# Performance work log

Measured on AMD Instinct MI355X. Metric: run time of the kernel, lower is better.

The kernel has to match this reference:

```python
import jax, jax.numpy as jnp
import numpy as np
import math

WINDOW = 512
N_HEAD = 16

def setup_inputs() -> dict:
    key = jax.random.key(0)
    ks = jax.random.split(key, 5)
    B, L, D = 2, 4096, 1024
    s = 0.02
    return {
        "x": jax.random.normal(ks[0], (B, L, D), dtype=jnp.float32),
        "Wq": jax.random.normal(ks[1], (D, D), dtype=jnp.float32) * s,
        "bq": jnp.zeros((D,), jnp.float32),
        "Wk": jax.random.normal(ks[2], (D, D), dtype=jnp.float32) * s,
        "bk": jnp.zeros((D,), jnp.float32),
        "Wv": jax.random.normal(ks[3], (D, D), dtype=jnp.float32) * s,
        "bv": jnp.zeros((D,), jnp.float32),
        "Wo": jax.random.normal(ks[4], (D, D), dtype=jnp.float32) * s,
        "bo": jnp.zeros((D,), jnp.float32),
    }

def reference(x, Wq, bq, Wk, bk, Wv, bv, Wo, bo):
    # Chunked sliding-window MHA (eval mode, dropout inactive).
    B, L, D = x.shape
    W, H = WINDOW, N_HEAD
    dh = D // H
    C = L // W  # number of query chunks
    scale = 1.0 / math.sqrt(dh)

    # Project full sequence once (linear, per-token -> identical math).
    q = x @ Wq.T + bq
    k = x @ Wk.T + bk
    v = x @ Wv.T + bv

    # Pad K/V by one window at the front so every chunk sees 2W keys.
    kp = jnp.pad(k, ((0, 0), (W, 0), (0, 0)))
    vp = jnp.pad(v, ((0, 0), (W, 0), (0, 0)))
    idx = jnp.arange(C)[:, None] * W + jnp.arange(2 * W)[None, :]  # [C, 2W] into padded seq
    kc = kp[:, idx].reshape(B, C, 2 * W, H, dh)
    vc = vp[:, idx].reshape(B, C, 2 * W, H, dh)
    qc = q.reshape(B, C, W, H, dh)

    scores = jnp.einsum('bcqhd,bckhd->bchqk', qc, kc) * scale  # [B,C,H,W,2W]
    valid = (idx >= W)  # padded positions (chunk 0's lookback) are invalid
    scores = jnp.where(valid[None, :, None, None, :], scores, jnp.float32(-1e9))
    attn = jax.nn.softmax(scores, axis=-1)
    out = jnp.einsum('bchqk,bckhd->bcqhd', attn, vc).reshape(B, L, D)
    return out @ Wo.T + bo
```

## Files before the change

kernel.cpp:

```cpp
#include <hip/hip_runtime.h>
#include <hip/hip_bf16.h>

typedef __hip_bfloat16 bf16;
typedef __attribute__((ext_vector_type(8))) short bf16x8;
typedef __attribute__((ext_vector_type(4))) float f32x4;
typedef unsigned int u32;
typedef unsigned short u16;

#define MFMA(a,b,c) __builtin_amdgcn_mfma_f32_16x16x32_bf16((a),(b),(c),0,0,0)

__device__ __forceinline__ u16 f32_to_bf16_rtne(float f) {
  u32 b = __builtin_bit_cast(u32, f);
  b += 0x7FFFu + ((b >> 16) & 1u);
  return (u16)(b >> 16);
}
__device__ __forceinline__ u32 pk2bf(float a, float b) {
  u32 ua = __builtin_bit_cast(u32, a); ua += 0x7FFFu + ((ua >> 16) & 1u);
  u32 ub = __builtin_bit_cast(u32, b); ub += 0x7FFFu + ((ub >> 16) & 1u);
  return __builtin_amdgcn_perm(ub, ua, 0x07060302u);
}
__device__ __forceinline__ u32 pk2bf_rtz(float a, float b) {
  return __builtin_amdgcn_perm(__builtin_bit_cast(u32, b),
                               __builtin_bit_cast(u32, a), 0x07060302u);
}
__device__ __forceinline__ uint4 cvt8(uint4 lo, uint4 hi) {
  const float4 fl = __builtin_bit_cast(float4, lo);
  const float4 fh = __builtin_bit_cast(float4, hi);
  uint4 r;
  r.x = pk2bf(fl.x, fl.y); r.y = pk2bf(fl.z, fl.w);
  r.z = pk2bf(fh.x, fh.y); r.w = pk2bf(fh.z, fh.w);
  return r;
}

__device__ __forceinline__ void barrier_lgkm() {
  asm volatile("s_waitcnt lgkmcnt(0)\n\ts_barrier" ::: "memory");
}

typedef const __attribute__((address_space(1))) void* gas_ptr;
typedef __attribute__((address_space(3))) void* las_ptr;
__device__ __forceinline__ void gload_lds16(const void* g, void* l) {
  __builtin_amdgcn_global_load_lds((gas_ptr)g, (las_ptr)l, 16, 0, 0);
}

static constexpr float SL2E = 0.125f * 1.44269504f;

__global__ __launch_bounds__(256)
void cast_all(const float* __restrict__ wq, const float* __restrict__ wk,
              const float* __restrict__ wv, const float* __restrict__ wo,
              const float* __restrict__ x,
              u16* __restrict__ wqkv, u16* __restrict__ wob,
              u16* __restrict__ xb) {
  const size_t DD8 = (size_t)1024 * 1024 / 8;
  if (blockIdx.x < 2048) {
    const int m = blockIdx.x >> 9;
    const size_t i = ((size_t)(blockIdx.x & 511)) * 256 + threadIdx.x;
    const float* src = (m == 0) ? wq : (m == 1) ? wk : (m == 2) ? wv : wo;
    u16* dst = (m < 3) ? (wqkv + (size_t)m * DD8 * 8) : wob;
    const float4* s = (const float4*)src + i * 2;
    ((uint4*)dst)[i] = cvt8(__builtin_bit_cast(uint4, s[0]),
                            __builtin_bit_cast(uint4, s[1]));
  } else {
    const size_t i = ((size_t)(blockIdx.x - 2048)) * 256 + threadIdx.x;
    const float4* s = (const float4*)x + i * 2;
    ((uint4*)xb)[i] = cvt8(__builtin_bit_cast(uint4, s[0]),
                           __builtin_bit_cast(uint4, s[1]));
  }
}

template <int MODE>
__global__ __launch_bounds__(256)
void gemm_bt(const bf16* __restrict__ A, const bf16* __restrict__ W,
             const float* __restrict__ b0, const float* __restrict__ b1,
             const float* __restrict__ b2, void* __restrict__ o0,
             void* __restrict__ o1, void* __restrict__ o2,
             int M, int N, int K)
{
  __shared__ bf16 As[128 * 64];
  __shared__ bf16 Bs[128 * 64];

  const int tid  = threadIdx.x;
  const int wave = tid >> 6, lane = tid & 63;
  const int quad = lane >> 4, l16 = lane & 15;
  const int wm   = wave >> 1, wn  = wave & 1;
  const int m0   = blockIdx.x * 128, n0 = blockIdx.y * 128;

  const int band = n0 >> 10;
  const float* bias = (band == 0) ? b0 : (band == 1) ? b1 : b2;

  const int srow = lane >> 3;
  const int sg   = lane & 7;
  const size_t rgs = (size_t)8 * K;
  const bf16* aSrc = A + (size_t)(m0 + wave * 32 + srow) * K + ((sg ^ srow) * 8);
  const bf16* wSrc = W + (size_t)(n0 + wave * 32 + srow) * K + ((sg ^ srow) * 8);
  bf16* aB = As + wave * 32 * 64;
  bf16* wB = Bs + wave * 32 * 64;

  const int niter = K >> 6;

  f32x4 acc[4][4] = {};

  const int arow[4] = { (wm * 64 + 0 * 16 + l16) * 64, (wm * 64 + 1 * 16 + l16) * 64,
                        (wm * 64 + 2 * 16 + l16) * 64, (wm * 64 + 3 * 16 + l16) * 64 };
  const int brow[4] = { (wn * 64 + 0 * 16 + l16) * 64, (wn * 64 + 1 * 16 + l16) * 64,
                        (wn * 64 + 2 * 16 + l16) * 64, (wn * 64 + 3 * 16 + l16) * 64 };
  const int r7 = l16 & 7;

  for (int t = 0; t < niter; ++t) {
    gload_lds16(aSrc,            aB);
    gload_lds16(aSrc + rgs,      aB + 512);
    gload_lds16(aSrc + 2 * rgs,  aB + 1024);
    gload_lds16(aSrc + 3 * rgs,  aB + 1536);
    gload_lds16(wSrc,            wB);
    gload_lds16(wSrc + rgs,      wB + 512);
    gload_lds16(wSrc + 2 * rgs,  wB + 1024);
    gload_lds16(wSrc + 3 * rgs,  wB + 1536);
    aSrc += 64; wSrc += 64;
    __syncthreads();

#pragma unroll
    for (int kk = 0; kk < 2; ++kk) {
      bf16x8 af[4], bw[4];
#pragma unroll
      for (int mt = 0; mt < 4; ++mt)
        af[mt] = *(const bf16x8*)(As + arow[mt] + (((kk * 4 + quad) ^ r7) * 8));
#pragma unroll
      for (int nt = 0; nt < 4; ++nt)
        bw[nt] = *(const bf16x8*)(Bs + brow[nt] + (((kk * 4 + quad) ^ r7) * 8));
#pragma unroll
      for (int mt = 0; mt < 4; ++mt)
#pragma unroll
        for (int nt = 0; nt < 4; ++nt)
          acc[mt][nt] = MFMA(af[mt], bw[nt], acc[mt][nt]);
    }
    if (t + 1 < niter) __syncthreads();
  }

#pragma unroll
  for (int nt = 0; nt < 4; ++nt) {
    const int col = n0 + wn * 64 + nt * 16 + l16;
    const int cl  = col & 1023;
    const float bv = bias[cl];
#pragma unroll
    for (int mt = 0; mt < 4; ++mt) {
      const int rbase = m0 + wm * 64 + mt * 16 + quad * 4;
      if (MODE == 1) {
#pragma unroll
        for (int r = 0; r < 4; ++r)
          ((float*)o0)[(size_t)(rbase + r) * N + col] = acc[mt][nt][r] + bv;
      } else if (band == 2) {
        const int hh = cl >> 6, dd = cl & 63;
        const int bb = rbase >> 12, tl = rbase & 4095;
        u16* dst = (u16*)o2 + ((size_t)((bb * 16 + hh) * 64 + dd)) * 4096 + tl;
        uint2 pk;
        pk.x = pk2bf(acc[mt][nt][0] + bv, acc[mt][nt][1] + bv);
        pk.y = pk2bf(acc[mt][nt][2] + bv, acc[mt][nt][3] + bv);
        *(uint2*)dst = pk;
      } else {
        u16* dst = (u16*)((band == 0) ? o0 : o1);
        const float sc = (band == 0) ? SL2E : 1.0f;
#pragma unroll
        for (int r = 0; r < 4; ++r)
          dst[(size_t)(rbase + r) * 1024 + cl] =
              f32_to_bf16_rtne((acc[mt][nt][r] + bv) * sc);
      }
    }
  }
}

__global__ __launch_bounds__(256)
void attn_swin(const bf16* __restrict__ qb, const bf16* __restrict__ kb,
               const bf16* __restrict__ vtb, u16* __restrict__ ctx)
{
  __shared__ __align__(16) bf16 Ks[2][64 * 72];
  __shared__ __align__(16) bf16 Vts[2][64 * 72];

  int bid = blockIdx.x;
  const int g  = bid & 255, qt = bid >> 8;
  const int h  = g & 15, c = (g >> 4) & 7, b = g >> 7;

  const int tid  = threadIdx.x;
  const int w    = tid >> 6, lane = tid & 63;
  const int quad = lane >> 4, l16 = lane & 15;

  const int tq0  = c * 512 + qt * 128;
  const int hoff = h * 64;
  const int kstart = (c == 0) ? 0 : (c - 1) * 512;
  const int nkt    = (c == 0) ? 8 : 16;

  bf16x8 qf[2][2];
#pragma unroll
  for (int u = 0; u < 2; ++u) {
    const bf16* qr = qb + ((size_t)(b * 4096 + tq0 + w * 32 + u * 16 + l16)) * 1024 + hoff;
    qf[u][0] = *(const bf16x8*)(qr + quad * 8);
    qf[u][1] = *(const bf16x8*)(qr + 32 + quad * 8);
  }

  const int m    = tid >> 2;
  const int cseg = (tid & 3) * 16;
  const int sig  = (((m >> 4) & 1) << 5) | (((m >> 2) & 3) << 3)
                 | (((m >> 5) & 1) << 2) | (m & 3);
  const bf16* kgp = kb + ((size_t)(b * 4096 + kstart + sig)) * 1024 + hoff + cseg;
  const bf16* vgp = vtb + ((size_t)((b * 16 + h) * 64 + m)) * 4096 + kstart + cseg;
  const int soff = m * 72 + cseg;

  float l_i[2] = {0.f, 0.f};
  f32x4 o[2][4] = {};

  uint4 ka0 = *(const uint4*)(kgp), ka1 = *(const uint4*)(kgp + 8);
  uint4 va0 = *(const uint4*)(vgp), va1 = *(const uint4*)(vgp + 8);
  kgp += (size_t)64 * 1024; vgp += 64;
  *(uint4*)(Ks[0] + soff) = ka0; *(uint4*)(Ks[0] + soff + 8) = ka1;
  *(uint4*)(Vts[0] + soff) = va0; *(uint4*)(Vts[0] + soff + 8) = va1;
  ka0 = *(const uint4*)(kgp); ka1 = *(const uint4*)(kgp + 8);
  va0 = *(const uint4*)(vgp); va1 = *(const uint4*)(vgp + 8);
  kgp += (size_t)64 * 1024; vgp += 64;
  barrier_lgkm();

  typedef union { u32 d[4]; bf16x8 v; } fragu;

  auto compute = [&](const bf16* ksb, const bf16* vtsb) {
    f32x4 s[2][4] = {};
#pragma unroll
    for (int kt = 0; kt < 4; ++kt) {
      const bf16* kr = ksb + (kt * 16 + l16) * 72;
      bf16x8 kf0 = *(const bf16x8*)(kr + quad * 8);
      bf16x8 kf1 = *(const bf16x8*)(kr + 32 + quad * 8);
      s[0][kt] = MFMA(kf0, qf[0][0], s[0][kt]);
      s[0][kt] = MFMA(kf1, qf[0][1], s[0][kt]);
      s[1][kt] = MFMA(kf0, qf[1][0], s[1][kt]);
      s[1][kt] = MFMA(kf1, qf[1][1], s[1][kt]);
    }
    fragu pf[2][2];
#pragma unroll
    for (int u = 0; u < 2; ++u) {
      float rs = 0.f;
#pragma unroll
      for (int kt = 0; kt < 4; ++kt)
#pragma unroll
        for (int r = 0; r < 4; ++r) {
          const float p = __builtin_amdgcn_exp2f(s[u][kt][r]);
          s[u][kt][r] = p;
          rs += p;
        }
      rs += __shfl_xor(rs, 16);
      rs += __shfl_xor(rs, 32);
      l_i[u] += rs;
#pragma unroll
      for (int hh = 0; hh < 2; ++hh)
#pragma unroll
        for (int dw = 0; dw < 4; ++dw) {
          const int kt = 2 * (dw >> 1) + hh, r0 = 2 * (dw & 1);
          pf[u][hh].d[dw] = pk2bf_rtz(s[u][kt][r0], s[u][kt][r0 + 1]);
        }
    }
#pragma unroll
    for (int dt = 0; dt < 4; ++dt) {
      const bf16* vr = vtsb + (dt * 16 + l16) * 72;
      bf16x8 vf0 = *(const bf16x8*)(vr + quad * 8);
      bf16x8 vf1 = *(const bf16x8*)(vr + 32 + quad * 8);
      o[0][dt] = MFMA(vf0, pf[0][0].v, o[0][dt]);
      o[0][dt] = MFMA(vf1, pf[0][1].v, o[0][dt]);
      o[1][dt] = MFMA(vf0, pf[1][0].v, o[1][dt]);
      o[1][dt] = MFMA(vf1, pf[1][1].v, o[1][dt]);
    }
  };

  for (int t = 0; t < nkt; t += 2) {
    *(uint4*)(Ks[1] + soff) = ka0; *(uint4*)(Ks[1] + soff + 8) = ka1;
    *(uint4*)(Vts[1] + soff) = va0; *(uint4*)(Vts[1] + soff + 8) = va1;
    if (t + 2 < nkt) {
      ka0 = *(const uint4*)(kgp); ka1 = *(const uint4*)(kgp + 8);
      va0 = *(const uint4*)(vgp); va1 = *(const uint4*)(vgp + 8);
      kgp += (size_t)64 * 1024; vgp += 64;
    }
    compute(Ks[0], Vts[0]);
    barrier_lgkm();

    if (t + 2 < nkt) {
      *(uint4*)(Ks[0] + soff) = ka0; *(uint4*)(Ks[0] + soff + 8) = ka1;
      *(uint4*)(Vts[0] + soff) = va0; *(uint4*)(Vts[0] + soff + 8) = va1;
      if (t + 3 < nkt) {
        ka0 = *(const uint4*)(kgp); ka1 = *(const uint4*)(kgp + 8);
        va0 = *(const uint4*)(vgp); va1 = *(const uint4*)(vgp + 8);
        kgp += (size_t)64 * 1024; vgp += 64;
      }
    }
    compute(Ks[1], Vts[1]);
    barrier_lgkm();
  }

#pragma unroll
  for (int u = 0; u < 2; ++u) {
    const float inv = 1.0f / l_i[u];
    const int qrow = tq0 + w * 32 + u * 16 + l16;
    u16* crow = ctx + ((size_t)(b * 4096 + qrow)) * 1024 + hoff;
#pragma unroll
    for (int dt = 0; dt < 4; ++dt) {
      uint2 pk;
      pk.x = pk2bf(o[u][dt][0] * inv, o[u][dt][1] * inv);
      pk.y = pk2bf(o[u][dt][2] * inv, o[u][dt][3] * inv);
      *(uint2*)(crow + dt * 16 + quad * 4) = pk;
    }
  }
}

extern "C" void kernel_launch(void* const* d_in, const int* in_sizes, int n_in,
                              void* d_out, int out_size, void* d_ws, size_t ws_size,
                              hipStream_t stream) {
  const float* x  = (const float*)d_in[0];
  const float* Wq = (const float*)d_in[1];
  const float* bq = (const float*)d_in[2];
  const float* Wk = (const float*)d_in[3];
  const float* bk = (const float*)d_in[4];
  const float* Wv = (const float*)d_in[5];
  const float* bv = (const float*)d_in[6];
  const float* Wo = (const float*)d_in[7];
  const float* bo = (const float*)d_in[8];

  const size_t MD = (size_t)8192 * 1024;
  const size_t DD = (size_t)1024 * 1024;

  char* ws = (char*)d_ws;
  u16*  Wqkvb = (u16*)ws;                     ws += 3 * DD * 2;
  u16*  Wob   = (u16*)ws;                     ws += DD * 2;
  u16*  qbuf  = (u16*)ws;                     ws += MD * 2;
  u16*  kbuf  = (u16*)ws;                     ws += MD * 2;
  u16*  vtb   = (u16*)ws;                     ws += MD * 2;
  u16*  ctx   = (u16*)ws;

  u16* xb = ctx;

  cast_all<<<dim3(6144), dim3(256), 0, stream>>>(Wq, Wk, Wv, Wo, x,
                                                 Wqkvb, Wob, xb);

  gemm_bt<0><<<dim3(64, 24), dim3(256), 0, stream>>>(
      (const bf16*)xb, (const bf16*)Wqkvb, bq, bk, bv,
      qbuf, kbuf, vtb, 8192, 3072, 1024);

  attn_swin<<<dim3(1024), dim3(256), 0, stream>>>(
      (const bf16*)qbuf, (const bf16*)kbuf, (const bf16*)vtb, ctx);

  gemm_bt<1><<<dim3(64, 8), dim3(256), 0, stream>>>(
      (const bf16*)ctx, (const bf16*)Wob, bo, bo, bo,
      d_out, nullptr, nullptr, 8192, 1024, 1024);
}
```

Measured before the change: 240.0 us.

## Replace QKV projection GEMM with 256x256-tile double-buffered pipelined kernel

Adds a new QKV projection kernel that uses 256x256 output tiles with 512 threads and double-buffered LDS filled by direct global-to-LDS loads two k-steps ahead. Each k-step is split into four phases with staggered prefetch issues, s_setprio around the MFMA bursts, and an XCD-aware workgroup remap. The aim is to raise arithmetic intensity and overlap memory with MFMA work in the largest GEMM. The cost is much higher LDS use (128KB per block) and register pressure, and only 384 workgroups, which risks lower occupancy. The output GEMM is split into its own specialised kernel.

Result: slower. 257.1 us (+7.1%).

```diff
diff --git a/kernel.cpp b/kernel.cpp
--- a/kernel.cpp
+++ b/kernel.cpp
@@ -34,6 +34,15 @@
 
 __device__ __forceinline__ void barrier_lgkm() {
   asm volatile("s_waitcnt lgkmcnt(0)\n\ts_barrier" ::: "memory");
+}
+__device__ __forceinline__ void barrier_plain() {
+  asm volatile("s_barrier" ::: "memory");
+}
+__device__ __forceinline__ void barrier_vm8() {
+  asm volatile("s_waitcnt vmcnt(8)\n\ts_barrier" ::: "memory");
+}
+__device__ __forceinline__ void barrier_vm0() {
+  asm volatile("s_waitcnt vmcnt(0)\n\ts_barrier" ::: "memory");
 }
 
 typedef const __attribute__((address_space(1))) void* gas_ptr;
@@ -67,13 +76,176 @@
   }
 }
 
-template <int MODE>
+__global__ __launch_bounds__(512, 2)
+void gemm256_qkv(const bf16* __restrict__ A, const bf16* __restrict__ W,
+                 const float* __restrict__ b0, const float* __restrict__ b1,
+                 const float* __restrict__ b2,
+                 u16* __restrict__ o0, u16* __restrict__ o1, u16* __restrict__ o2,
+                 int M, int N, int K)
+{
+  __shared__ bf16 AsB[2][256 * 64];
+  __shared__ bf16 BsB[2][256 * 64];
+
+  int wg = blockIdx.y * gridDim.x + blockIdx.x;
+  const int q8 = (gridDim.x * gridDim.y) >> 3;
+  wg = (wg & 7) * q8 + (wg >> 3);
+  const int bx = wg & 31;
+  const int by = wg >> 5;
+  const int m0 = bx * 256, n0 = by * 256;
+
+  const int tid  = threadIdx.x;
+  const int wv   = tid >> 6, lane = tid & 63;
+  const int quad = lane >> 4, l16 = lane & 15;
+  const int wm   = wv >> 2, wn = wv & 3;
+  const int r7   = l16 & 7;
+
+  const int rr = tid >> 3, g = tid & 7;
+  const int sg8 = (g ^ (rr & 7)) * 8;
+  const bf16* aS = A + (size_t)(m0 + rr) * K + sg8;
+  const bf16* wS = W + (size_t)(n0 + rr) * K + sg8;
+  const int ldstW = wv * 8 * 64;
+
+#define STA(c, qk, kt) gload_lds16(aS + ((size_t)(qk) * 64) * K + (kt) * 64, \
+                                   &AsB[c][(qk) * 64 * 64 + ldstW])
+#define STB(c, qk, kt) gload_lds16(wS + ((size_t)(qk) * 64) * K + (kt) * 64, \
+                                   &BsB[c][(qk) * 64 * 64 + ldstW])
+
+  int aoff[8], boff[4];
+#pragma unroll
+  for (int mt = 0; mt < 8; ++mt) aoff[mt] = (wm * 128 + mt * 16 + l16) * 64;
+#pragma unroll
+  for (int nt = 0; nt < 4; ++nt) boff[nt] = (wn * 64 + nt * 16 + l16) * 64;
+  const int k0 = (quad ^ r7) * 8;
+  const int k1 = ((4 + quad) ^ r7) * 8;
+
+  f32x4 acc[8][4] = {};
+  bf16x8 af[4][2], bl[2][2], bh[2][2];
+
+  const int nk = K >> 6;
+
+#pragma unroll
+  for (int qk = 0; qk < 4; ++qk) { STA(0, qk, 0); STB(0, qk, 0); }
+#pragma unroll
+  for (int qk = 0; qk < 4; ++qk) { STA(1, qk, 1); STB(1, qk, 1); }
+  barrier_vm8();
+
+  for (int t = 0; t < nk; ++t) {
+    const int c = t & 1;
+    const bf16* Ac = AsB[c];
+    const bf16* Bc = BsB[c];
+    const int t2 = t + 2;
+    const bool pf = (t2 < nk);
+
+#pragma unroll
+    for (int mt = 0; mt < 4; ++mt) {
+      af[mt][0] = *(const bf16x8*)(Ac + aoff[mt] + k0);
+      af[mt][1] = *(const bf16x8*)(Ac + aoff[mt] + k1);
+    }
+#pragma unroll
+    for (int nt = 0; nt < 2; ++nt) {
+      bl[nt][0] = *(const bf16x8*)(Bc + boff[nt] + k0);
+      bl[nt][1] = *(const bf16x8*)(Bc + boff[nt] + k1);
+    }
+    barrier_plain();
+    __builtin_amdgcn_s_setprio(1);
+#pragma unroll
+    for (int mt = 0; mt < 4; ++mt)
+#pragma unroll
+      for (int nt = 0; nt < 2; ++nt) {
+        acc[mt][nt] = MFMA(af[mt][0], bl[nt][0], acc[mt][nt]);
+        acc[mt][nt] = MFMA(af[mt][1], bl[nt][1], acc[mt][nt]);
+      }
+    __builtin_amdgcn_s_setprio(0);
+    barrier_lgkm();
+
+#pragma unroll
+    for (int nt = 0; nt < 2; ++nt) {
+      bh[nt][0] = *(const bf16x8*)(Bc + boff[nt + 2] + k0);
+      bh[nt][1] = *(const bf16x8*)(Bc + boff[nt + 2] + k1);
+    }
+    if (pf) { STA(c, 0, t2); STA(c, 2, t2); }
+    barrier_plain();
+    __builtin_amdgcn_s_setprio(1);
+#pragma unroll
+    for (int mt = 0; mt < 4; ++mt)
+#pragma unroll
+      for (int nt = 0; nt < 2; ++nt) {
+        acc[mt][nt + 2] = MFMA(af[mt][0], bh[nt][0], acc[mt][nt + 2]);
+        acc[mt][nt + 2] = MFMA(af[mt][1], bh[nt][1], acc[mt][nt + 2]);
+      }
+    __builtin_amdgcn_s_setprio(0);
+    barrier_lgkm();
+
+#pragma unroll
+    for (int mt = 0; mt < 4; ++mt) {
+      af[mt][0] = *(const bf16x8*)(Ac + aoff[mt + 4] + k0);
+      af[mt][1] = *(const bf16x8*)(Ac + aoff[mt + 4] + k1);
+    }
+    if (pf) { STB(c, 0, t2); STB(c, 1, t2); }
+    barrier_plain();
+    __builtin_amdgcn_s_setprio(1);
+#pragma unroll
+    for (int mt = 0; mt < 4; ++mt)
+#pragma unroll
+      for (int nt = 0; nt < 2; ++nt) {
+        acc[mt + 4][nt + 2] = MFMA(af[mt][0], bh[nt][0], acc[mt + 4][nt + 2]);
+        acc[mt + 4][nt + 2] = MFMA(af[mt][1], bh[nt][1], acc[mt + 4][nt + 2]);
+      }
+    __builtin_amdgcn_s_setprio(0);
+    barrier_lgkm();
+
+    if (pf) { STA(c, 1, t2); STA(c, 3, t2); STB(c, 2, t2); STB(c, 3, t2); }
+    barrier_plain();
+    __builtin_amdgcn_s_setprio(1);
+#pragma unroll
+    for (int mt = 0; mt < 4; ++mt)
+#pragma unroll
+      for (int nt = 0; nt < 2; ++nt) {
+        acc[mt + 4][nt] = MFMA(af[mt][0], bl[nt][0], acc[mt + 4][nt]);
+        acc[mt + 4][nt] = MFMA(af[mt][1], bl[nt][1], acc[mt + 4][nt]);
+      }
+    __builtin_amdgcn_s_setprio(0);
+    if (t + 1 < nk) {
+      if (pf) barrier_vm8(); else barrier_vm0();
+    }
+  }
+#undef STA
+#undef STB
+
+  const int band = n0 >> 10;
+  const float* bias = (band == 0) ? b0 : (band == 1) ? b1 : b2;
+#pragma unroll
+  for (int nt = 0; nt < 4; ++nt) {
+    const int col = n0 + wn * 64 + nt * 16 + l16;
+    const int cl  = col & 1023;
+    const float bv = bias[cl];
+#pragma unroll
+    for (int mt = 0; mt < 8; ++mt) {
+      const int rbase = m0 + wm * 128 + mt * 16 + quad * 4;
+      if (band == 2) {
+        const int hh = cl >> 6, dd = cl & 63;
+        const int bb = rbase >> 12, tl = rbase & 4095;
+        u16* dst = o2 + ((size_t)((bb * 16 + hh) * 64 + dd)) * 4096 + tl;
+        uint2 pk;
+        pk.x = pk2bf(acc[mt][nt][0] + bv, acc[mt][nt][1] + bv);
+        pk.y = pk2bf(acc[mt][nt][2] + bv, acc[mt][nt][3] + bv);
+        *(uint2*)dst = pk;
+      } else {
+        u16* dst = (band == 0) ? o0 : o1;
+        const float sc = (band == 0) ? SL2E : 1.0f;
+#pragma unroll
+        for (int r = 0; r < 4; ++r)
+          dst[(size_t)(rbase + r) * 1024 + cl] =
+              f32_to_bf16_rtne((acc[mt][nt][r] + bv) * sc);
+      }
+    }
+  }
+}
+
 __global__ __launch_bounds__(256)
-void gemm_bt(const bf16* __restrict__ A, const bf16* __restrict__ W,
-             const float* __restrict__ b0, const float* __restrict__ b1,
-             const float* __restrict__ b2, void* __restrict__ o0,
-             void* __restrict__ o1, void* __restrict__ o2,
-             int M, int N, int K)
+void gemm_out(const bf16* __restrict__ A, const bf16* __restrict__ W,
+              const float* __restrict__ bias, float* __restrict__ out,
+              int M, int N, int K)
 {
   __shared__ bf16 As[128 * 64];
   __shared__ bf16 Bs[128 * 64];
@@ -83,9 +255,6 @@
   const int quad = lane >> 4, l16 = lane & 15;
   const int wm   = wave >> 1, wn  = wave & 1;
   const int m0   = blockIdx.x * 128, n0 = blockIdx.y * 128;
-
-  const int band = n0 >> 10;
-  const float* bias = (band == 0) ? b0 : (band == 1) ? b1 : b2;
 
   const int srow = lane >> 3;
   const int sg   = lane & 7;
@@ -138,31 +307,13 @@
 #pragma unroll
   for (int nt = 0; nt < 4; ++nt) {
     const int col = n0 + wn * 64 + nt * 16 + l16;
-    const int cl  = col & 1023;
-    const float bv = bias[cl];
+    const float bv = bias[col & 1023];
 #pragma unroll
     for (int mt = 0; mt < 4; ++mt) {
       const int rbase = m0 + wm * 64 + mt * 16 + quad * 4;
-      if (MODE == 1) {
-#pragma unroll
-        for (int r = 0; r < 4; ++r)
-          ((float*)o0)[(size_t)(rbase + r) * N + col] = acc[mt][nt][r] + bv;
-      } else if (band == 2) {
-        const int hh = cl >> 6, dd = cl & 63;
-        const int bb = rbase >> 12, tl = rbase & 4095;
-        u16* dst = (u16*)o2 + ((size_t)((bb * 16 + hh) * 64 + dd)) * 4096 + tl;
-        uint2 pk;
-        pk.x = pk2bf(acc[mt][nt][0] + bv, acc[mt][nt][1] + bv);
-        pk.y = pk2bf(acc[mt][nt][2] + bv, acc[mt][nt][3] + bv);
-        *(uint2*)dst = pk;
-      } else {
-        u16* dst = (u16*)((band == 0) ? o0 : o1);
-        const float sc = (band == 0) ? SL2E : 1.0f;
-#pragma unroll
-        for (int r = 0; r < 4; ++r)
-          dst[(size_t)(rbase + r) * 1024 + cl] =
-              f32_to_bf16_rtne((acc[mt][nt][r] + bv) * sc);
-      }
+#pragma unroll
+      for (int r = 0; r < 4; ++r)
+        out[(size_t)(rbase + r) * N + col] = acc[mt][nt][r] + bv;
     }
   }
 }
@@ -333,14 +484,13 @@
   cast_all<<<dim3(6144), dim3(256), 0, stream>>>(Wq, Wk, Wv, Wo, x,
                                                  Wqkvb, Wob, xb);
 
-  gemm_bt<0><<<dim3(64, 24), dim3(256), 0, stream>>>(
+  gemm256_qkv<<<dim3(32, 12), dim3(512), 0, stream>>>(
       (const bf16*)xb, (const bf16*)Wqkvb, bq, bk, bv,
       qbuf, kbuf, vtb, 8192, 3072, 1024);
 
   attn_swin<<<dim3(1024), dim3(256), 0, stream>>>(
       (const bf16*)qbuf, (const bf16*)kbuf, (const bf16*)vtb, ctx);
 
-  gemm_bt<1><<<dim3(64, 8), dim3(256), 0, stream>>>(
-      (const bf16*)ctx, (const bf16*)Wob, bo, bo, bo,
-      d_out, nullptr, nullptr, 8192, 1024, 1024);
-}
+  gemm_out<<<dim3(64, 8), dim3(256), 0, stream>>>(
+      (const bf16*)ctx, (const bf16*)Wob, bo, (float*)d_out, 8192, 1024, 1024);
+}
```

## Rewrite GEMMs as 8-wave 128x256 tiles with double-buffered LDS pipelining

Applied to the files above, without the earlier changes.

Replaces the single-buffered 128x128, 4-wave GEMM with a 512-thread kernel that computes 128x256 tiles. A and B tiles are double-buffered in LDS and prefetched one to two k-steps ahead, and each step is split into two MFMA phases with raised wave priority. It also adds an XCD-aware remap of workgroup IDs. The aim is to hide global-load latency behind MFMA work and to reuse the larger tile better, at the cost of more LDS per block, subtle waitcnt/barrier ordering, and fewer workgroups.

Result: no change. 244.7 us (+2.0%).

```diff
diff --git a/kernel.cpp b/kernel.cpp
--- a/kernel.cpp
+++ b/kernel.cpp
@@ -34,6 +34,9 @@
 
 __device__ __forceinline__ void barrier_lgkm() {
   asm volatile("s_waitcnt lgkmcnt(0)\n\ts_barrier" ::: "memory");
+}
+__device__ __forceinline__ void barrier_plain() {
+  asm volatile("s_barrier" ::: "memory");
 }
 
 typedef const __attribute__((address_space(1))) void* gas_ptr;
@@ -68,73 +71,120 @@
 }
 
 template <int MODE>
-__global__ __launch_bounds__(256)
-void gemm_bt(const bf16* __restrict__ A, const bf16* __restrict__ W,
-             const float* __restrict__ b0, const float* __restrict__ b1,
-             const float* __restrict__ b2, void* __restrict__ o0,
-             void* __restrict__ o1, void* __restrict__ o2,
-             int M, int N, int K)
+__global__ __launch_bounds__(512, 2)
+void gemm8p(const bf16* __restrict__ A, const bf16* __restrict__ W,
+            const float* __restrict__ b0, const float* __restrict__ b1,
+            const float* __restrict__ b2, void* __restrict__ o0,
+            void* __restrict__ o1, void* __restrict__ o2,
+            int M, int N, int K)
 {
-  __shared__ bf16 As[128 * 64];
-  __shared__ bf16 Bs[128 * 64];
+  __shared__ __align__(16) bf16 AsB[2][128 * 64];
+  __shared__ __align__(16) bf16 BsB[2][256 * 64];
+
+  const int nwg = gridDim.x * gridDim.y;
+  const int raw = blockIdx.y * gridDim.x + blockIdx.x;
+  const int vwg = (raw & 7) * (nwg >> 3) + (raw >> 3);
+  const int NT  = gridDim.y;
+  const int bx  = vwg / NT, by = vwg - bx * NT;
+  const int m0  = bx * 128, n0 = by * 256;
 
   const int tid  = threadIdx.x;
-  const int wave = tid >> 6, lane = tid & 63;
+  const int wv   = tid >> 6, lane = tid & 63;
   const int quad = lane >> 4, l16 = lane & 15;
-  const int wm   = wave >> 1, wn  = wave & 1;
-  const int m0   = blockIdx.x * 128, n0 = blockIdx.y * 128;
+  const int wm   = wv >> 2, wn = wv & 3;
+  const int r7   = l16 & 7;
+
+  const int rr = tid >> 3, g = tid & 7;
+  const int sg8 = (g ^ (rr & 7)) * 8;
+  const bf16* aS = A + (size_t)(m0 + rr) * K + sg8;
+  const bf16* wS = W + (size_t)(n0 + rr) * K + sg8;
+  const int ldstW = wv * 512;
+
+#define STA8(buf, kt) do { \
+    gload_lds16(aS + (size_t)(kt) * 64,                      &AsB[buf][ldstW]); \
+    gload_lds16(aS + (size_t)64 * K + (size_t)(kt) * 64,     &AsB[buf][4096 + ldstW]); \
+  } while (0)
+#define STB8(buf, kt) do { \
+    gload_lds16(wS + (size_t)(kt) * 64,                      &BsB[buf][ldstW]); \
+    gload_lds16(wS + (size_t)64 * K + (size_t)(kt) * 64,     &BsB[buf][4096 + ldstW]); \
+    gload_lds16(wS + (size_t)128 * K + (size_t)(kt) * 64,    &BsB[buf][8192 + ldstW]); \
+    gload_lds16(wS + (size_t)192 * K + (size_t)(kt) * 64,    &BsB[buf][12288 + ldstW]); \
+  } while (0)
+
+  int aoff[4], boff[4];
+#pragma unroll
+  for (int mt = 0; mt < 4; ++mt) aoff[mt] = (wm * 64 + mt * 16 + l16) * 64;
+#pragma unroll
+  for (int nt = 0; nt < 4; ++nt) boff[nt] = (wn * 64 + nt * 16 + l16) * 64;
+  const int k0o = (quad ^ r7) * 8;
+  const int k1o = ((4 + quad) ^ r7) * 8;
+
+  f32x4 acc[4][4] = {};
+  bf16x8 bfr[4][2], afr[2][2];
+
+  const int nk = K >> 6;
+
+  STA8(0, 0);
+  STB8(0, 0);
+  STB8(1, 1);
+  asm volatile("s_waitcnt vmcnt(4)\n\ts_barrier" ::: "memory");
+
+  for (int t = 0; t < nk; ++t) {
+    const int c = t & 1;
+    const bf16* Ac = AsB[c];
+    const bf16* Bc = BsB[c];
+
+#pragma unroll
+    for (int nt = 0; nt < 4; ++nt) {
+      bfr[nt][0] = *(const bf16x8*)(Bc + boff[nt] + k0o);
+      bfr[nt][1] = *(const bf16x8*)(Bc + boff[nt] + k1o);
+    }
+#pragma unroll
+    for (int mt = 0; mt < 2; ++mt) {
+      afr[mt][0] = *(const bf16x8*)(Ac + aoff[mt] + k0o);
+      afr[mt][1] = *(const bf16x8*)(Ac + aoff[mt] + k1o);
+    }
+    if (t + 1 < nk) STA8((t + 1) & 1, t + 1);
+    barrier_plain();
+    __builtin_amdgcn_s_setprio(1);
+#pragma unroll
+    for (int mt = 0; mt < 2; ++mt)
+#pragma unroll
+      for (int nt = 0; nt < 4; ++nt) {
+        acc[mt][nt] = MFMA(afr[mt][0], bfr[nt][0], acc[mt][nt]);
+        acc[mt][nt] = MFMA(afr[mt][1], bfr[nt][1], acc[mt][nt]);
+      }
+    __builtin_amdgcn_s_setprio(0);
+    barrier_lgkm();
+
+#pragma unroll
+    for (int mt = 0; mt < 2; ++mt) {
+      afr[mt][0] = *(const bf16x8*)(Ac + aoff[mt + 2] + k0o);
+      afr[mt][1] = *(const bf16x8*)(Ac + aoff[mt + 2] + k1o);
+    }
+    if (t + 2 < nk) STB8(c, t + 2);
+    barrier_plain();
+    __builtin_amdgcn_s_setprio(1);
+#pragma unroll
+    for (int mt = 0; mt < 2; ++mt)
+#pragma unroll
+      for (int nt = 0; nt < 4; ++nt) {
+        acc[mt + 2][nt] = MFMA(afr[mt][0], bfr[nt][0], acc[mt + 2][nt]);
+        acc[mt + 2][nt] = MFMA(afr[mt][1], bfr[nt][1], acc[mt + 2][nt]);
+      }
+    __builtin_amdgcn_s_setprio(0);
+    if (t + 1 < nk) {
+      if (t + 2 < nk)
+        asm volatile("s_waitcnt vmcnt(4) lgkmcnt(0)\n\ts_barrier" ::: "memory");
+      else
+        asm volatile("s_waitcnt vmcnt(0) lgkmcnt(0)\n\ts_barrier" ::: "memory");
+    }
+  }
+#undef STA8
+#undef STB8
 
   const int band = n0 >> 10;
   const float* bias = (band == 0) ? b0 : (band == 1) ? b1 : b2;
-
-  const int srow = lane >> 3;
-  const int sg   = lane & 7;
-  const size_t rgs = (size_t)8 * K;
-  const bf16* aSrc = A + (size_t)(m0 + wave * 32 + srow) * K + ((sg ^ srow) * 8);
-  const bf16* wSrc = W + (size_t)(n0 + wave * 32 + srow) * K + ((sg ^ srow) * 8);
-  bf16* aB = As + wave * 32 * 64;
-  bf16* wB = Bs + wave * 32 * 64;
-
-  const int niter = K >> 6;
-
-  f32x4 acc[4][4] = {};
-
-  const int arow[4] = { (wm * 64 + 0 * 16 + l16) * 64, (wm * 64 + 1 * 16 + l16) * 64,
-                        (wm * 64 + 2 * 16 + l16) * 64, (wm * 64 + 3 * 16 + l16) * 64 };
-  const int brow[4] = { (wn * 64 + 0 * 16 + l16) * 64, (wn * 64 + 1 * 16 + l16) * 64,
-                        (wn * 64 + 2 * 16 + l16) * 64, (wn * 64 + 3 * 16 + l16) * 64 };
-  const int r7 = l16 & 7;
-
-  for (int t = 0; t < niter; ++t) {
-    gload_lds16(aSrc,            aB);
-    gload_lds16(aSrc + rgs,      aB + 512);
-    gload_lds16(aSrc + 2 * rgs,  aB + 1024);
-    gload_lds16(aSrc + 3 * rgs,  aB + 1536);
-    gload_lds16(wSrc,            wB);
-    gload_lds16(wSrc + rgs,      wB + 512);
-    gload_lds16(wSrc + 2 * rgs,  wB + 1024);
-    gload_lds16(wSrc + 3 * rgs,  wB + 1536);
-    aSrc += 64; wSrc += 64;
-    __syncthreads();
-
-#pragma unroll
-    for (int kk = 0; kk < 2; ++kk) {
-      bf16x8 af[4], bw[4];
-#pragma unroll
-      for (int mt = 0; mt < 4; ++mt)
-        af[mt] = *(const bf16x8*)(As + arow[mt] + (((kk * 4 + quad) ^ r7) * 8));
-#pragma unroll
-      for (int nt = 0; nt < 4; ++nt)
-        bw[nt] = *(const bf16x8*)(Bs + brow[nt] + (((kk * 4 + quad) ^ r7) * 8));
-#pragma unroll
-      for (int mt = 0; mt < 4; ++mt)
-#pragma unroll
-        for (int nt = 0; nt < 4; ++nt)
-          acc[mt][nt] = MFMA(af[mt], bw[nt], acc[mt][nt]);
-    }
-    if (t + 1 < niter) __syncthreads();
-  }
-
 #pragma unroll
   for (int nt = 0; nt < 4; ++nt) {
     const int col = n0 + wn * 64 + nt * 16 + l16;
@@ -333,14 +383,14 @@
   cast_all<<<dim3(6144), dim3(256), 0, stream>>>(Wq, Wk, Wv, Wo, x,
                                                  Wqkvb, Wob, xb);
 
-  gemm_bt<0><<<dim3(64, 24), dim3(256), 0, stream>>>(
+  gemm8p<0><<<dim3(64, 12), dim3(512), 0, stream>>>(
       (const bf16*)xb, (const bf16*)Wqkvb, bq, bk, bv,
       qbuf, kbuf, vtb, 8192, 3072, 1024);
 
   attn_swin<<<dim3(1024), dim3(256), 0, stream>>>(
       (const bf16*)qbuf, (const bf16*)kbuf, (const bf16*)vtb, ctx);
 
-  gemm_bt<1><<<dim3(64, 8), dim3(256), 0, stream>>>(
+  gemm8p<1><<<dim3(64, 4), dim3(512), 0, stream>>>(
       (const bf16*)ctx, (const bf16*)Wob, bo, bo, bo,
       d_out, nullptr, nullptr, 8192, 1024, 1024);
 }
```
